# Kernel optimization log

Hardware: AMD Instinct MI355X
Metric: run time of the kernel (lower is better)

Reference implementation:

```python
import jax, jax.numpy as jnp
import numpy as np

E = 1024  # embedding_dim
H = 64    # head_size

def setup_inputs() -> dict:
    key = jax.random.key(0)
    k1, k2, k3, k4 = jax.random.split(key, 4)
    x = jax.random.normal(k1, (4, 4096, E), dtype=jnp.float32)
    # nn.Linear(E, H, bias=False) weights have shape [H, E]; y = x @ W.T
    s = 1.0 / np.sqrt(E)
    Wq = jax.random.normal(k2, (H, E), dtype=jnp.float32) * s
    Wk = jax.random.normal(k3, (H, E), dtype=jnp.float32) * s
    Wv = jax.random.normal(k4, (H, E), dtype=jnp.float32) * s
    return {"x": x, "Wq": Wq, "Wk": Wk, "Wv": Wv}

def reference(x, Wq, Wk, Wv):
    B, T, E_ = x.shape
    q = jnp.einsum('bte,he->bth', x, Wq)
    k = jnp.einsum('bte,he->bth', x, Wk)
    v = jnp.einsum('bte,he->bth', x, Wv)
    # NOTE: original scales by sqrt(embedding_dim), not head_size
    scores = jnp.einsum('bqh,bkh->bqk', q, k) / jnp.sqrt(jnp.asarray(E_, x.dtype))
    causal = jnp.tril(jnp.ones((T, T), dtype=bool))
    scores = jnp.where(causal, scores, -jnp.inf)
    weights = jax.nn.softmax(scores, axis=-1)
    return jnp.einsum('bqk,bkh->bqh', weights, v)
```

## Files before the change

kernel.cpp:

```cpp
#include <hip/hip_runtime.h>
#include <stdint.h>

typedef __bf16 bf16x8 __attribute__((ext_vector_type(8)));
typedef float  f32x4  __attribute__((ext_vector_type(4)));

#define E_DIM 1024
#define H_DIM 64
#define T_SEQ 4096
#define B_BAT 4
#define M_TOT (B_BAT * T_SEQ)
#define NSPLIT 8

__device__ __forceinline__ uint32_t f2bf1(float f) {
    uint32_t u = __float_as_uint(f);
    return (u + 0x7FFFu + ((u >> 16) & 1u)) >> 16;
}
__device__ __forceinline__ uint32_t pk2(float lo, float hi) {
    return f2bf1(lo) | (f2bf1(hi) << 16);
}
__device__ __forceinline__ bf16x8 ldfrag(const ushort* p) {
    return __builtin_bit_cast(bf16x8, *(const uint4*)(p));
}
__device__ __forceinline__ float bf2f(uint32_t u) {
    return __uint_as_float(u << 16);
}
__device__ __forceinline__ void barrier_lgkm() {
    __builtin_amdgcn_s_waitcnt(0xC07F);
    __builtin_amdgcn_s_barrier();
}

__global__ __launch_bounds__(256) void wcvt(const float* __restrict__ Wq,
                                            const float* __restrict__ Wk,
                                            const float* __restrict__ Wv,
                                            ushort* __restrict__ Wfm) {
    int g = blockIdx.x * 256 + threadIdx.x;
    int n = g >> 7;
    int k8 = g & 127;
    const float* src = (n < 64) ? (Wq + (size_t)n * E_DIM)
                     : (n < 128) ? (Wk + (size_t)(n - 64) * E_DIM)
                     : (Wv + (size_t)(n - 128) * E_DIM);
    float sc = (n < 64) ? 0.04508422f : 1.0f;
    float4 a = *(const float4*)(src + k8 * 8);
    float4 b = *(const float4*)(src + k8 * 8 + 4);
    uint4 o;
    o.x = pk2(a.x * sc, a.y * sc); o.y = pk2(a.z * sc, a.w * sc);
    o.z = pk2(b.x * sc, b.y * sc); o.w = pk2(b.z * sc, b.w * sc);
    int s = k8 >> 3, kc = (k8 >> 2) & 1, qd = k8 & 3;
    int nt = n >> 4, lm = n & 15;
    int lane = qd * 16 + lm;
    *(uint4*)(Wfm + (((size_t)(s * 12 + nt) * 2 + kc) * 64 + lane) * 8) = o;
}

__global__ __launch_bounds__(256, 3) void qkv(const float* __restrict__ x,
                                              const ushort* __restrict__ Wfm,
                                              ushort* __restrict__ Qfm,
                                              ushort* __restrict__ Kfm,
                                              ushort* __restrict__ Vfm) {
    __shared__ union {
        ushort a[2][32 * 72];
        struct { ushort c[32 * 136]; ushort vt[64 * 40]; } epi;
    } sm;
    const int tid = threadIdx.x;
    const int w = tid >> 6, l = tid & 63;
    const int lm = l & 15, qd = l >> 4;
    const int m0 = blockIdx.x * 32;

    f32x4 acc[2][3];
#pragma unroll
    for (int r2 = 0; r2 < 2; ++r2)
#pragma unroll
        for (int t = 0; t < 3; ++t) acc[r2][t] = (f32x4){0.f, 0.f, 0.f, 0.f};

    const int srow = tid >> 3, kseg = tid & 7;
    const float* xsrc = x + (size_t)(m0 + srow) * E_DIM + kseg * 8;

    {
        float4 a0 = *(const float4*)xsrc;
        float4 a1 = *(const float4*)(xsrc + 4);
        uint4 u = {pk2(a0.x, a0.y), pk2(a0.z, a0.w), pk2(a1.x, a1.y), pk2(a1.z, a1.w)};
        *(uint4*)(&sm.a[0][srow * 72 + kseg * 8]) = u;
    }
    float4 xn0 = *(const float4*)(xsrc + 64);
    float4 xn1 = *(const float4*)(xsrc + 68);
    __syncthreads();

    for (int s = 0; s < 16; ++s) {
        const int cb = s & 1, nb = cb ^ 1;
        float4 x20 = xn0, x21 = xn1;
        if (s < 14) {
            x20 = *(const float4*)(xsrc + (s + 2) * 64);
            x21 = *(const float4*)(xsrc + (s + 2) * 64 + 4);
        }
        bf16x8 wf[3][2];
#pragma unroll
        for (int t = 0; t < 3; ++t)
#pragma unroll
            for (int kc = 0; kc < 2; ++kc)
                wf[t][kc] = ldfrag(Wfm + (((size_t)(s * 12 + w * 3 + t) * 2 + kc) * 64 + l) * 8);
        bf16x8 af[2][2];
#pragma unroll
        for (int r2 = 0; r2 < 2; ++r2)
#pragma unroll
            for (int kc = 0; kc < 2; ++kc)
                af[r2][kc] = ldfrag(&sm.a[cb][(r2 * 16 + lm) * 72 + kc * 32 + qd * 8]);
#pragma unroll
        for (int t = 0; t < 3; ++t)
#pragma unroll
            for (int kc = 0; kc < 2; ++kc)
#pragma unroll
                for (int r2 = 0; r2 < 2; ++r2)
                    acc[r2][t] = __builtin_amdgcn_mfma_f32_16x16x32_bf16(af[r2][kc], wf[t][kc], acc[r2][t], 0, 0, 0);
        if (s < 15) {
            uint4 u = {pk2(xn0.x, xn0.y), pk2(xn0.z, xn0.w), pk2(xn1.x, xn1.y), pk2(xn1.z, xn1.w)};
            *(uint4*)(&sm.a[nb][srow * 72 + kseg * 8]) = u;
        }
        xn0 = x20; xn1 = x21;
        if (s < 15) barrier_lgkm();
    }
    __syncthreads();

#pragma unroll
    for (int r2 = 0; r2 < 2; ++r2)
#pragma unroll
        for (int t = 0; t < 3; ++t) {
            int gc = w * 48 + t * 16 + lm;
            int m = r2 * 16 + qd * 4;
#pragma unroll
            for (int rr = 0; rr < 4; ++rr) {
                ushort v = (ushort)f2bf1(acc[r2][t][rr]);
                if (gc < 128) sm.epi.c[(m + rr) * 136 + gc] = v;
                else          sm.epi.vt[(gc - 128) * 40 + (m + rr)] = v;
            }
        }
    __syncthreads();

    const int g16b = m0 >> 4;
    const int kt64 = m0 >> 6;
    const int tb   = (m0 >> 4) & 3;
    const int kcv  = (m0 >> 5) & 1;
#pragma unroll
    for (int ii = 0; ii < 3; ++ii) {
        int i = w + ii * 4;
        uint4 val;
        ushort* dst;
        if (i < 4) {
            int qt_l = i >> 1, kc = i & 1;
            val = *(const uint4*)(&sm.epi.c[(qt_l * 16 + lm) * 136 + kc * 32 + qd * 8]);
            dst = Qfm + (((size_t)(g16b + qt_l) * 2 + kc) * 64 + l) * 8;
        } else if (i < 8) {
            int j2 = i - 4, t_l = j2 >> 1, kc = j2 & 1;
            val = *(const uint4*)(&sm.epi.c[(t_l * 16 + lm) * 136 + 64 + kc * 32 + qd * 8]);
            dst = Kfm + (((size_t)((kt64 * 4 + tb + t_l) * 2 + kc)) * 64 + l) * 8;
        } else {
            int t = i - 8;
            val = *(const uint4*)(&sm.epi.vt[(t * 16 + lm) * 40 + qd * 8]);
            dst = Vfm + (((size_t)((kt64 * 4 + t) * 2 + kcv)) * 64 + l) * 8;
        }
        *(uint4*)dst = val;
    }
}

__global__ __launch_bounds__(256, 4) void flash(const ushort* __restrict__ Qfm,
                                                const ushort* __restrict__ Kfm,
                                                const ushort* __restrict__ Vfm,
                                                ushort* __restrict__ Opart,
                                                float* __restrict__ lpart) {
    __shared__ ushort plds[4][16 * 72];
    const int tid = threadIdx.x;
    const int wv = tid >> 6, l = tid & 63;
    const int lm = l & 15, qd = l >> 4;
    const int pr = blockIdx.x;
    const int bt = blockIdx.y;
    const int h  = blockIdx.z;
    ushort* myp = plds[wv];

#pragma unroll 1
    for (int half = 0; half < 2; ++half) {
        const int qt = half ? (63 - pr) : pr;
        const size_t rowg = (size_t)bt * T_SEQ + qt * 64 + wv * 16;
        const int g16 = bt * 256 + qt * 4 + wv;

        bf16x8 qf0, qf1;
        {
            const ushort* qp = Qfm + ((size_t)g16 * 2) * 512 + l * 8;
            qf0 = ldfrag(qp);
            qf1 = ldfrag(qp + 512);
        }
        f32x4 o[4];
#pragma unroll
        for (int t = 0; t < 4; ++t) o[t] = (f32x4){0.f, 0.f, 0.f, 0.f};
        float lacc = 0.f;

#pragma unroll 1
        for (int kt = h; kt <= qt; kt += NSPLIT) {
            const ushort* kb = Kfm + ((size_t)(bt * 64 + kt) * 8) * 512;
            const ushort* vb = Vfm + ((size_t)(bt * 64 + kt) * 8) * 512;
            f32x4 sf[4];
#pragma unroll
            for (int t = 0; t < 4; ++t) sf[t] = (f32x4){0.f, 0.f, 0.f, 0.f};
#pragma unroll
            for (int t = 0; t < 4; ++t) {
                bf16x8 k0 = ldfrag(kb + (t * 2 + 0) * 512 + l * 8);
                bf16x8 k1 = ldfrag(kb + (t * 2 + 1) * 512 + l * 8);
                sf[t] = __builtin_amdgcn_mfma_f32_16x16x32_bf16(k0, qf0, sf[t], 0, 0, 0);
                sf[t] = __builtin_amdgcn_mfma_f32_16x16x32_bf16(k1, qf1, sf[t], 0, 0, 0);
            }
            uint4 vu[4][2];
#pragma unroll
            for (int t = 0; t < 4; ++t) {
                vu[t][0] = *(const uint4*)(vb + (t * 2 + 0) * 512 + l * 8);
                vu[t][1] = *(const uint4*)(vb + (t * 2 + 1) * 512 + l * 8);
            }
            ushort* wp = myp + lm * 72 + qd * 4;
            if (kt != qt) {
#pragma unroll
                for (int t = 0; t < 4; ++t) {
                    float p0 = exp2f(sf[t][0]), p1 = exp2f(sf[t][1]);
                    float p2 = exp2f(sf[t][2]), p3 = exp2f(sf[t][3]);
                    lacc += (p0 + p1) + (p2 + p3);
                    *(uint2*)(wp + t * 16) = uint2{pk2(p0, p1), pk2(p2, p3)};
                }
            } else {
#pragma unroll
                for (int t = 0; t < 4; ++t) {
                    if (t < wv) {
                        float p0 = exp2f(sf[t][0]), p1 = exp2f(sf[t][1]);
                        float p2 = exp2f(sf[t][2]), p3 = exp2f(sf[t][3]);
                        lacc += (p0 + p1) + (p2 + p3);
                        *(uint2*)(wp + t * 16) = uint2{pk2(p0, p1), pk2(p2, p3)};
                    } else if (t == wv) {
                        float p[4];
#pragma unroll
                        for (int rr = 0; rr < 4; ++rr) {
                            float pe = exp2f(sf[t][rr]);
                            if (qd * 4 + rr > lm) pe = 0.f;
                            lacc += pe;
                            p[rr] = pe;
                        }
                        *(uint2*)(wp + t * 16) = uint2{pk2(p[0], p[1]), pk2(p[2], p[3])};
                    } else {
                        *(uint2*)(wp + t * 16) = uint2{0u, 0u};
                    }
                }
            }
            __builtin_amdgcn_wave_barrier();
            __builtin_amdgcn_s_waitcnt(0xC07F);
            __builtin_amdgcn_wave_barrier();
            bf16x8 pf0 = ldfrag(myp + lm * 72 + qd * 8);
            bf16x8 pf1 = ldfrag(myp + lm * 72 + 32 + qd * 8);
#pragma unroll
            for (int t = 0; t < 4; ++t) {
                bf16x8 v0 = __builtin_bit_cast(bf16x8, vu[t][0]);
                bf16x8 v1 = __builtin_bit_cast(bf16x8, vu[t][1]);
                o[t] = __builtin_amdgcn_mfma_f32_16x16x32_bf16(pf0, v0, o[t], 0, 0, 0);
                o[t] = __builtin_amdgcn_mfma_f32_16x16x32_bf16(pf1, v1, o[t], 0, 0, 0);
            }
            __builtin_amdgcn_wave_barrier();
        }
        lacc += __shfl_xor(lacc, 16);
        lacc += __shfl_xor(lacc, 32);

        ushort* ob = Opart + ((size_t)h * M_TOT + rowg) * 64;
#pragma unroll
        for (int t = 0; t < 4; ++t)
#pragma unroll
            for (int rr = 0; rr < 4; ++rr)
                ob[(size_t)(qd * 4 + rr) * 64 + t * 16 + lm] = (ushort)f2bf1(o[t][rr]);
        if (qd == 0) lpart[(size_t)h * M_TOT + rowg + lm] = lacc;
    }
}

__global__ __launch_bounds__(256) void combine(const ushort* __restrict__ Opart,
                                               const float* __restrict__ lpart,
                                               float* __restrict__ out) {
    int i4 = blockIdx.x * 256 + threadIdx.x;
    size_t base = (size_t)i4 * 4;
    int row = i4 >> 4;
    float ls = 0.f;
#pragma unroll
    for (int j = 0; j < NSPLIT; ++j) ls += lpart[(size_t)j * M_TOT + row];
    float s0 = 0.f, s1 = 0.f, s2 = 0.f, s3 = 0.f;
    const size_t SP = (size_t)M_TOT * 64;
#pragma unroll
    for (int j = 0; j < NSPLIT; ++j) {
        uint2 u = *(const uint2*)(Opart + (size_t)j * SP + base);
        s0 += bf2f(u.x & 0xFFFFu); s1 += bf2f(u.x >> 16);
        s2 += bf2f(u.y & 0xFFFFu); s3 += bf2f(u.y >> 16);
    }
    float inv = 1.0f / ls;
    float4 o = {s0 * inv, s1 * inv, s2 * inv, s3 * inv};
    *(float4*)(out + base) = o;
}

extern "C" void kernel_launch(void* const* d_in, const int* in_sizes, int n_in,
                              void* d_out, int out_size, void* d_ws, size_t ws_size,
                              hipStream_t stream) {
    const float* x  = (const float*)d_in[0];
    const float* Wq = (const float*)d_in[1];
    const float* Wk = (const float*)d_in[2];
    const float* Wv = (const float*)d_in[3];
    float* out = (float*)d_out;

    char* ws = (char*)d_ws;
    ushort* Wfm = (ushort*)(ws);
    ushort* Qfm = (ushort*)(ws + 393216);
    ushort* Kfm = (ushort*)(ws + 2490368);
    ushort* Vfm = (ushort*)(ws + 4587520);
    ushort* Op  = (ushort*)(ws + 6684672);
    float*  lp  = (float*) (ws + 23461888);

    wcvt<<<96, 256, 0, stream>>>(Wq, Wk, Wv, Wfm);
    qkv<<<512, 256, 0, stream>>>(x, Wfm, Qfm, Kfm, Vfm);
    flash<<<dim3(32, B_BAT, NSPLIT), 256, 0, stream>>>(Qfm, Kfm, Vfm, Op, lp);
    combine<<<1024, 256, 0, stream>>>(Op, lp, out);
}
```

Before: 137.7 us.

## Remap flash blocks per XCD and store partial outputs in fragment layout

The flash kernel now uses a 1D grid and decodes block index so that blocks of the same batch land on the same XCD (blocks are dispatched round-robin across XCDs), improving L2 reuse of K/V. Partial outputs are written as packed 16-byte fragment-ordered vectors instead of scattered 2-byte stores. The combine kernel is rewritten to read this fragment layout and write rows, at the cost of less coalesced fp32 output stores.

New measurement: 137.0 us. Within noise of the previous version (-0.5%).

```diff
diff --git a/kernel.cpp b/kernel.cpp
--- a/kernel.cpp
+++ b/kernel.cpp
@@ -20,6 +20,9 @@
 }
 __device__ __forceinline__ bf16x8 ldfrag(const ushort* p) {
     return __builtin_bit_cast(bf16x8, *(const uint4*)(p));
+}
+__device__ __forceinline__ bf16x8 u2f(uint4 u) {
+    return __builtin_bit_cast(bf16x8, u);
 }
 __device__ __forceinline__ float bf2f(uint32_t u) {
     return __uint_as_float(u << 16);
@@ -169,15 +172,17 @@
     const int tid = threadIdx.x;
     const int wv = tid >> 6, l = tid & 63;
     const int lm = l & 15, qd = l >> 4;
-    const int pr = blockIdx.x;
-    const int bt = blockIdx.y;
-    const int h  = blockIdx.z;
+    const int lin = blockIdx.x;
+    const int xcd = lin & 7;
+    const int bt = xcd >> 1;
+    const int rest = lin >> 3;
+    const int pr = rest & 31;
+    const int h = ((rest >> 5) << 1) | (xcd & 1);
     ushort* myp = plds[wv];
 
 #pragma unroll 1
     for (int half = 0; half < 2; ++half) {
         const int qt = half ? (63 - pr) : pr;
-        const size_t rowg = (size_t)bt * T_SEQ + qt * 64 + wv * 16;
         const int g16 = bt * 256 + qt * 4 + wv;
 
         bf16x8 qf0, qf1;
@@ -250,46 +255,68 @@
             bf16x8 pf1 = ldfrag(myp + lm * 72 + 32 + qd * 8);
 #pragma unroll
             for (int t = 0; t < 4; ++t) {
-                bf16x8 v0 = __builtin_bit_cast(bf16x8, vu[t][0]);
-                bf16x8 v1 = __builtin_bit_cast(bf16x8, vu[t][1]);
-                o[t] = __builtin_amdgcn_mfma_f32_16x16x32_bf16(pf0, v0, o[t], 0, 0, 0);
-                o[t] = __builtin_amdgcn_mfma_f32_16x16x32_bf16(pf1, v1, o[t], 0, 0, 0);
+                o[t] = __builtin_amdgcn_mfma_f32_16x16x32_bf16(pf0, u2f(vu[t][0]), o[t], 0, 0, 0);
+                o[t] = __builtin_amdgcn_mfma_f32_16x16x32_bf16(pf1, u2f(vu[t][1]), o[t], 0, 0, 0);
             }
             __builtin_amdgcn_wave_barrier();
         }
         lacc += __shfl_xor(lacc, 16);
         lacc += __shfl_xor(lacc, 32);
 
-        ushort* ob = Opart + ((size_t)h * M_TOT + rowg) * 64;
-#pragma unroll
-        for (int t = 0; t < 4; ++t)
-#pragma unroll
-            for (int rr = 0; rr < 4; ++rr)
-                ob[(size_t)(qd * 4 + rr) * 64 + t * 16 + lm] = (ushort)f2bf1(o[t][rr]);
-        if (qd == 0) lpart[(size_t)h * M_TOT + rowg + lm] = lacc;
+        ushort* ob = Opart + (((size_t)h * 1024 + g16) * 2) * 512 + l * 8;
+        uint4 A = {pk2(o[0][0], o[0][1]), pk2(o[0][2], o[0][3]),
+                   pk2(o[1][0], o[1][1]), pk2(o[1][2], o[1][3])};
+        uint4 B = {pk2(o[2][0], o[2][1]), pk2(o[2][2], o[2][3]),
+                   pk2(o[3][0], o[3][1]), pk2(o[3][2], o[3][3])};
+        *(uint4*)ob = A;
+        *(uint4*)(ob + 512) = B;
+        if (qd == 0) lpart[(size_t)h * M_TOT + g16 * 16 + lm] = lacc;
     }
 }
 
 __global__ __launch_bounds__(256) void combine(const ushort* __restrict__ Opart,
                                                const float* __restrict__ lpart,
                                                float* __restrict__ out) {
-    int i4 = blockIdx.x * 256 + threadIdx.x;
-    size_t base = (size_t)i4 * 4;
-    int row = i4 >> 4;
-    float ls = 0.f;
-#pragma unroll
-    for (int j = 0; j < NSPLIT; ++j) ls += lpart[(size_t)j * M_TOT + row];
-    float s0 = 0.f, s1 = 0.f, s2 = 0.f, s3 = 0.f;
-    const size_t SP = (size_t)M_TOT * 64;
+    const int tid = threadIdx.x;
+    const int wv = tid >> 6, l = tid & 63;
+    const int lm = l & 15, qd = l >> 4;
+    const int g16 = blockIdx.x * 4 + wv;
+
+    float s[4][4];
+#pragma unroll
+    for (int t = 0; t < 4; ++t)
+#pragma unroll
+        for (int rr = 0; rr < 4; ++rr) s[t][rr] = 0.f;
 #pragma unroll
     for (int j = 0; j < NSPLIT; ++j) {
-        uint2 u = *(const uint2*)(Opart + (size_t)j * SP + base);
-        s0 += bf2f(u.x & 0xFFFFu); s1 += bf2f(u.x >> 16);
-        s2 += bf2f(u.y & 0xFFFFu); s3 += bf2f(u.y >> 16);
-    }
-    float inv = 1.0f / ls;
-    float4 o = {s0 * inv, s1 * inv, s2 * inv, s3 * inv};
-    *(float4*)(out + base) = o;
+        const ushort* pb = Opart + (((size_t)j * 1024 + g16) * 2) * 512 + l * 8;
+        uint4 a = *(const uint4*)pb;
+        uint4 b = *(const uint4*)(pb + 512);
+        s[0][0] += bf2f(a.x & 0xFFFFu); s[0][1] += bf2f(a.x >> 16);
+        s[0][2] += bf2f(a.y & 0xFFFFu); s[0][3] += bf2f(a.y >> 16);
+        s[1][0] += bf2f(a.z & 0xFFFFu); s[1][1] += bf2f(a.z >> 16);
+        s[1][2] += bf2f(a.w & 0xFFFFu); s[1][3] += bf2f(a.w >> 16);
+        s[2][0] += bf2f(b.x & 0xFFFFu); s[2][1] += bf2f(b.x >> 16);
+        s[2][2] += bf2f(b.y & 0xFFFFu); s[2][3] += bf2f(b.y >> 16);
+        s[3][0] += bf2f(b.z & 0xFFFFu); s[3][1] += bf2f(b.z >> 16);
+        s[3][2] += bf2f(b.w & 0xFFFFu); s[3][3] += bf2f(b.w >> 16);
+    }
+    float inv[4];
+#pragma unroll
+    for (int rr = 0; rr < 4; ++rr) {
+        float ls = 0.f;
+#pragma unroll
+        for (int j = 0; j < NSPLIT; ++j)
+            ls += lpart[(size_t)j * M_TOT + g16 * 16 + qd * 4 + rr];
+        inv[rr] = 1.0f / ls;
+    }
+#pragma unroll
+    for (int rr = 0; rr < 4; ++rr) {
+        size_t row = (size_t)g16 * 16 + qd * 4 + rr;
+#pragma unroll
+        for (int t = 0; t < 4; ++t)
+            out[row * 64 + t * 16 + lm] = s[t][rr] * inv[rr];
+    }
 }
 
 extern "C" void kernel_launch(void* const* d_in, const int* in_sizes, int n_in,
@@ -311,6 +338,6 @@
 
     wcvt<<<96, 256, 0, stream>>>(Wq, Wk, Wv, Wfm);
     qkv<<<512, 256, 0, stream>>>(x, Wfm, Qfm, Kfm, Vfm);
-    flash<<<dim3(32, B_BAT, NSPLIT), 256, 0, stream>>>(Qfm, Kfm, Vfm, Op, lp);
-    combine<<<1024, 256, 0, stream>>>(Op, lp, out);
-}
+    flash<<<1024, 256, 0, stream>>>(Qfm, Kfm, Vfm, Op, lp);
+    combine<<<256, 256, 0, stream>>>(Op, lp, out);
+}
```
